# Kernel optimization log

Hardware: AMD Instinct MI355X
Metric: run time of the kernel (lower is better)

The kernel has to match this reference:

```python
import jax, jax.numpy as jnp
import numpy as np

B = 524288   # batch rows
K = 8        # number of BooleanClassifiers
I = 64       # n_inputs
H = 32       # n_hidden
SCALE = 1.0  # LinearNetwork.scale (default [1.0])


def setup_inputs() -> dict:
    key = jax.random.key(0)
    k_x, k_w1, k_b1, k_w2, k_b2 = jax.random.split(key, 5)
    return {
        "x": jax.random.normal(k_x, (B, I), dtype=jnp.float32),
        "W1": jax.random.normal(k_w1, (K, H, I), dtype=jnp.float32) * 0.1,
        "b1": jax.random.normal(k_b1, (K, H), dtype=jnp.float32) * 0.1,
        "W2": jax.random.normal(k_w2, (K, H), dtype=jnp.float32) * 0.1,
        "b2": jax.random.normal(k_b2, (K,), dtype=jnp.float32) * 0.1,
        "bias": jnp.zeros((K,), dtype=jnp.float32),  # unused in training-mode forward
    }


def reference(x, W1, b1, W2, b2, bias):
    # Loop of K tiny Linear-Tanh-Linear-Tanh classifiers, fused as batched GEMMs.
    # h: [B, K, H]
    h = jnp.tanh(jnp.einsum("bi,khi->bkh", x, W1) + b1)
    # per-classifier scalar output, concatenated along dim=1 -> [B, K]
    out = jnp.tanh(jnp.einsum("bkh,kh->bk", h, W2) + b2)
    out = out * SCALE                   # LinearNetwork scale
    out = (out + 1.0) * 0.5 * SCALE     # LinearWithTanh training branch
    return out
```

## Files before the change

kernel.cpp:

```cpp
#include <hip/hip_runtime.h>

typedef __attribute__((ext_vector_type(8))) short short8;
typedef __attribute__((ext_vector_type(4))) float f32x4;

constexpr int B_ROWS   = 524288;
constexpr int ROWTILES = B_ROWS / 64;
constexpr int GRID     = 2048;
constexpr int ITERS    = ROWTILES / GRID;
constexpr float L2E2   = 2.8853900817779268f;

union V16 { uint4 u; short8 s; };

__device__ __forceinline__ unsigned pk(float lo, float hi) {
  const unsigned a = __float_as_uint(lo) + 0x8000u;
  const unsigned b = __float_as_uint(hi) + 0x8000u;
  return __builtin_amdgcn_perm(b, a, 0x07060302u);
}

__device__ __forceinline__ V16 pk8(f32x4 a, f32x4 b) {
  V16 v;
  v.u.x = pk(a[0], a[1]); v.u.y = pk(a[2], a[3]);
  v.u.z = pk(b[0], b[1]); v.u.w = pk(b[2], b[3]);
  return v;
}

__global__ __launch_bounds__(256, 4) void fused_mlp8(
    const float* __restrict__ x, const float* __restrict__ W1,
    const float* __restrict__ b1, const float* __restrict__ W2,
    const float* __restrict__ b2, float* __restrict__ out) {

  __shared__ V16  xb[2][512];
  __shared__ float ob[2][64 * 10];

  const int tid  = threadIdx.x;
  const int wave = tid >> 6;
  const int lane = tid & 63;
  const int m16  = lane & 15;
  const int q    = lane >> 4;

  short8 w1f[4][2];
#pragma unroll
  for (int mt = 0; mt < 4; ++mt) {
    const int n = (wave * 4 + mt) * 16 + m16;
#pragma unroll
    for (int ks = 0; ks < 2; ++ks) {
      const float* p = W1 + n * 64 + ks * 32 + q * 8;
      const f32x4 u0 = *(const f32x4*)p, u1 = *(const f32x4*)(p + 4);
      f32x4 s0, s1;
#pragma unroll
      for (int r = 0; r < 4; ++r) { s0[r] = L2E2 * u0[r]; s1[r] = L2E2 * u1[r]; }
      w1f[mt][ks] = pk8(s0, s1).s;
    }
  }

  f32x4 kb1[4], w2m[4];
  float sw2[2] = {0.f, 0.f};
#pragma unroll
  for (int mt = 0; mt < 4; ++mt) {
    const int n0 = (wave * 4 + mt) * 16 + q * 4;
    const f32x4 b1x = *(const f32x4*)(b1 + n0);
    const f32x4 w2x = *(const f32x4*)(W2 + n0);
#pragma unroll
    for (int r = 0; r < 4; ++r) {
      kb1[mt][r] = L2E2 * b1x[r];
      w2m[mt][r] = -2.0f * w2x[r];
      sw2[mt >> 1] += w2x[r];
    }
  }
  float KSb[2];
#pragma unroll
  for (int j = 0; j < 2; ++j) {
    float s = sw2[j];
    s += __shfl_xor(s, 16);
    s += __shfl_xor(s, 32);
    KSb[j] = L2E2 * (s + b2[wave * 2 + j]);
  }

  const int srow = tid >> 2;
  const int seg  = tid & 3;
  const int sw   = srow & 7;
  const float* gbase = x + (long)srow * 64 + seg * 16;

  f32x4 pf[4];
#pragma unroll
  for (int c = 0; c < 4; ++c)
    pf[c] = *(const f32x4*)(gbase + (long)blockIdx.x * 4096 + c * 4);
  xb[0][srow * 8 + ((seg * 2)     ^ sw)] = pk8(pf[0], pf[1]);
  xb[0][srow * 8 + ((seg * 2 + 1) ^ sw)] = pk8(pf[2], pf[3]);
#pragma unroll
  for (int c = 0; c < 4; ++c)
    pf[c] = *(const f32x4*)(gbase + ((long)blockIdx.x + GRID) * 4096 + c * 4);
  __syncthreads();

#pragma unroll
  for (int i = 0; i < ITERS; ++i) {
    const int p = i & 1;
    const long tile = (long)blockIdx.x + (long)i * GRID;

#pragma unroll
    for (int tt = 0; tt < 4; ++tt) {
      const int r   = tt * 16 + m16;
      const int rsw = r & 7;
      const short8 xf0 = xb[p][r * 8 + (q       ^ rsw)].s;
      const short8 xf1 = xb[p][r * 8 + ((q + 4) ^ rsw)].s;

      f32x4 acc[4];
#pragma unroll
      for (int mt = 0; mt < 4; ++mt) {
        f32x4 z = { 0.f, 0.f, 0.f, 0.f };
        z = __builtin_amdgcn_mfma_f32_16x16x32_bf16(w1f[mt][0], xf0, z, 0, 0, 0);
        z = __builtin_amdgcn_mfma_f32_16x16x32_bf16(w1f[mt][1], xf1, z, 0, 0, 0);
        acc[mt] = z;
      }

      float o0 = 0.f, o1 = 0.f;
#pragma unroll
      for (int j = 0; j < 2; ++j) {
        float P = 0.f;
#pragma unroll
        for (int t = 0; t < 2; ++t) {
          const int mt = j * 2 + t;
#pragma unroll
          for (int rr = 0; rr < 4; ++rr) {
            const float e = __builtin_amdgcn_exp2f(acc[mt][rr] + kb1[mt][rr]);
            P = __builtin_fmaf(w2m[mt][rr], __builtin_amdgcn_rcpf(e + 1.0f), P);
          }
        }
        P += __shfl_xor(P, 16);
        P += __shfl_xor(P, 32);
        const float arg = __builtin_fmaf(P, L2E2, KSb[j]);
        const float o = 1.0f - __builtin_amdgcn_rcpf(
            __builtin_amdgcn_exp2f(arg) + 1.0f);
        if (j == 0) o0 = o; else o1 = o;
      }

      if (q == 0) {
        float2 st; st.x = o0; st.y = o1;
        *(float2*)&ob[p][r * 10 + wave * 2] = st;
      }
    }

    if (i + 1 < ITERS) {
      xb[p ^ 1][srow * 8 + ((seg * 2)     ^ sw)] = pk8(pf[0], pf[1]);
      xb[p ^ 1][srow * 8 + ((seg * 2 + 1) ^ sw)] = pk8(pf[2], pf[3]);
    }

    __syncthreads();

    {
      const int orow = tid >> 2, oc = (tid & 3) * 2;
      const float2 v = *(const float2*)&ob[p][orow * 10 + oc];
      *(float2*)(out + (tile * 64 + orow) * 8 + oc) = v;
    }

    if (i + 2 < ITERS) {
      const float* gp = gbase + (tile + 2 * GRID) * 4096;
#pragma unroll
      for (int c = 0; c < 4; ++c) pf[c] = *(const f32x4*)(gp + c * 4);
    }
  }
}

extern "C" void kernel_launch(void* const* d_in, const int* in_sizes, int n_in,
                              void* d_out, int out_size, void* d_ws, size_t ws_size,
                              hipStream_t stream) {
  const float* x  = (const float*)d_in[0];
  const float* W1 = (const float*)d_in[1];
  const float* b1 = (const float*)d_in[2];
  const float* W2 = (const float*)d_in[3];
  const float* b2 = (const float*)d_in[4];
  float* out = (float*)d_out;
  fused_mlp8<<<GRID, 256, 0, stream>>>(x, W1, b1, W2, b2, out);
}
```

Baseline: 207.3 us.

## Pair sigmoid reciprocals, fold bias into MFMA, move final tanh to store phase

Combines two hidden-unit sigmoid terms over a common denominator so each pair needs one reciprocal instead of two. Seeds the MFMA accumulator with the scaled b1, removing a per-element add. Replaces the second cross-lane shuffle with two partial sums written to shared memory, and moves the final tanh into the cooperative store phase so each output is computed by one thread. Also halves the grid so each block runs more iterations. The pairing trades one rcp for extra multiplies and may lose range if exp2 values overflow in the product.

```diff
diff --git a/kernel.cpp b/kernel.cpp
--- a/kernel.cpp
+++ b/kernel.cpp
@@ -5,7 +5,7 @@
 
 constexpr int B_ROWS   = 524288;
 constexpr int ROWTILES = B_ROWS / 64;
-constexpr int GRID     = 2048;
+constexpr int GRID     = 1024;
 constexpr int ITERS    = ROWTILES / GRID;
 constexpr float L2E2   = 2.8853900817779268f;
 
@@ -30,7 +30,8 @@
     const float* __restrict__ b2, float* __restrict__ out) {
 
   __shared__ V16  xb[2][512];
-  __shared__ float ob[2][64 * 10];
+  __shared__ float ob[2][64 * 18];
+  __shared__ float kshare[8];
 
   const int tid  = threadIdx.x;
   const int wave = tid >> 6;
@@ -67,19 +68,19 @@
       sw2[mt >> 1] += w2x[r];
     }
   }
-  float KSb[2];
 #pragma unroll
   for (int j = 0; j < 2; ++j) {
     float s = sw2[j];
     s += __shfl_xor(s, 16);
     s += __shfl_xor(s, 32);
-    KSb[j] = L2E2 * (s + b2[wave * 2 + j]);
+    if (lane == 0) kshare[wave * 2 + j] = L2E2 * (s + b2[wave * 2 + j]);
   }
 
   const int srow = tid >> 2;
   const int seg  = tid & 3;
   const int sw   = srow & 7;
   const float* gbase = x + (long)srow * 64 + seg * 16;
+  const int orow = tid >> 2, oc = (tid & 3) * 2;
 
   f32x4 pf[4];
 #pragma unroll
@@ -91,6 +92,8 @@
   for (int c = 0; c < 4; ++c)
     pf[c] = *(const f32x4*)(gbase + ((long)blockIdx.x + GRID) * 4096 + c * 4);
   __syncthreads();
+
+  const float KS0 = kshare[oc], KS1 = kshare[oc + 1];
 
 #pragma unroll
   for (int i = 0; i < ITERS; ++i) {
@@ -107,13 +110,13 @@
       f32x4 acc[4];
 #pragma unroll
       for (int mt = 0; mt < 4; ++mt) {
-        f32x4 z = { 0.f, 0.f, 0.f, 0.f };
+        f32x4 z = kb1[mt];
         z = __builtin_amdgcn_mfma_f32_16x16x32_bf16(w1f[mt][0], xf0, z, 0, 0, 0);
         z = __builtin_amdgcn_mfma_f32_16x16x32_bf16(w1f[mt][1], xf1, z, 0, 0, 0);
         acc[mt] = z;
       }
 
-      float o0 = 0.f, o1 = 0.f;
+      float P0 = 0.f, P1 = 0.f;
 #pragma unroll
       for (int j = 0; j < 2; ++j) {
         float P = 0.f;
@@ -121,22 +124,24 @@
         for (int t = 0; t < 2; ++t) {
           const int mt = j * 2 + t;
 #pragma unroll
-          for (int rr = 0; rr < 4; ++rr) {
-            const float e = __builtin_amdgcn_exp2f(acc[mt][rr] + kb1[mt][rr]);
-            P = __builtin_fmaf(w2m[mt][rr], __builtin_amdgcn_rcpf(e + 1.0f), P);
+          for (int pr = 0; pr < 2; ++pr) {
+            const float ta = 1.0f + __builtin_amdgcn_exp2f(acc[mt][pr * 2]);
+            const float tb = 1.0f + __builtin_amdgcn_exp2f(acc[mt][pr * 2 + 1]);
+            const float N  = __builtin_fmaf(w2m[mt][pr * 2], tb,
+                                            w2m[mt][pr * 2 + 1] * ta);
+            P = __builtin_fmaf(N, __builtin_amdgcn_rcpf(ta * tb), P);
           }
         }
         P += __shfl_xor(P, 16);
-        P += __shfl_xor(P, 32);
-        const float arg = __builtin_fmaf(P, L2E2, KSb[j]);
-        const float o = 1.0f - __builtin_amdgcn_rcpf(
-            __builtin_amdgcn_exp2f(arg) + 1.0f);
-        if (j == 0) o0 = o; else o1 = o;
+        if (j == 0) P0 = P; else P1 = P;
       }
-
       if (q == 0) {
-        float2 st; st.x = o0; st.y = o1;
-        *(float2*)&ob[p][r * 10 + wave * 2] = st;
+        float2 st; st.x = P0; st.y = P1;
+        *(float2*)&ob[p][r * 18 + wave * 2] = st;
+      }
+      if (q == 2) {
+        float2 st; st.x = P0; st.y = P1;
+        *(float2*)&ob[p][r * 18 + 8 + wave * 2] = st;
       }
     }
 
@@ -148,9 +153,14 @@
     __syncthreads();
 
     {
-      const int orow = tid >> 2, oc = (tid & 3) * 2;
-      const float2 v = *(const float2*)&ob[p][orow * 10 + oc];
-      *(float2*)(out + (tile * 64 + orow) * 8 + oc) = v;
+      const float2 ha = *(const float2*)&ob[p][orow * 18 + oc];
+      const float2 hb = *(const float2*)&ob[p][orow * 18 + 8 + oc];
+      const float a0 = __builtin_fmaf(ha.x + hb.x, L2E2, KS0);
+      const float a1 = __builtin_fmaf(ha.y + hb.y, L2E2, KS1);
+      float2 o;
+      o.x = 1.0f - __builtin_amdgcn_rcpf(__builtin_amdgcn_exp2f(a0) + 1.0f);
+      o.y = 1.0f - __builtin_amdgcn_rcpf(__builtin_amdgcn_exp2f(a1) + 1.0f);
+      *(float2*)(out + (tile * 64 + orow) * 8 + oc) = o;
     }
 
     if (i + 2 < ITERS) {
```

Result: slower. 213.4 us (+3.0%).
